# Kernel optimization log

Hardware: AMD Instinct MI355X
Metric: run time of the kernel (lower is better)

Reference implementation:

```python
import jax, jax.numpy as jnp
import numpy as np

N_NODES = 100000
N_EDGES = 200000
N_GRAPHS = 4000
F_IN = 44
H = 256
E = 512
L = 4


def setup_inputs() -> dict:
    key = jax.random.key(0)
    ks = jax.random.split(key, 16)
    x = jax.random.normal(ks[0], (N_NODES, F_IN), dtype=jnp.float32)
    edge_index = jax.random.randint(ks[1], (2, N_EDGES), 0, N_NODES)
    batch = jnp.sort(jax.random.randint(ks[2], (N_NODES,), 0, N_GRAPHS))
    s = lambda fan_in: 1.0 / np.sqrt(fan_in)
    W_atom = jax.random.uniform(ks[3], (F_IN, H), jnp.float32, -s(F_IN), s(F_IN))
    b_atom = jnp.zeros((H,), jnp.float32)
    W1 = jax.random.uniform(ks[4], (L, H, 2 * H), jnp.float32, -s(H), s(H))
    b1 = jnp.zeros((L, 2 * H), jnp.float32)
    W2 = jax.random.uniform(ks[5], (L, 2 * H, H), jnp.float32, -s(2 * H), s(2 * H))
    b2 = jnp.zeros((L, H), jnp.float32)
    Wf1 = jax.random.uniform(ks[6], (H, H), jnp.float32, -s(H), s(H))
    bf1 = jnp.zeros((H,), jnp.float32)
    Wf2 = jax.random.uniform(ks[7], (H, E), jnp.float32, -s(H), s(H))
    bf2 = jnp.zeros((E,), jnp.float32)
    return {"x": x, "edge_index": edge_index, "batch": batch,
            "W_atom": W_atom, "b_atom": b_atom,
            "W1": W1, "b1": b1, "W2": W2, "b2": b2,
            "Wf1": Wf1, "bf1": bf1, "Wf2": Wf2, "bf2": bf2}


def reference(x, edge_index, batch, W_atom, b_atom, W1, b1, W2, b2, Wf1, bf1, Wf2, bf2):
    src, dst = edge_index[0], edge_index[1]
    h = jax.nn.relu(x @ W_atom + b_atom)  # [N, H]
    for l in range(L):
        # GIN aggregation: agg_i = sum_{j->i} h_j ; eps=0 so node term is h_i itself
        agg = jax.ops.segment_sum(h[src], dst, num_segments=N_NODES)
        z = h + agg
        z = jax.nn.relu(z @ W1[l] + b1[l])
        z = z @ W2[l] + b2[l]
        h = jax.nn.relu(z)
    # global mean pool by graph id
    sums = jax.ops.segment_sum(h, batch, num_segments=N_GRAPHS)
    counts = jax.ops.segment_sum(jnp.ones((N_NODES,), h.dtype), batch, num_segments=N_GRAPHS)
    h_graph = sums / jnp.maximum(counts, 1.0)[:, None]  # [G, H]
    out = jax.nn.relu(h_graph @ Wf1 + bf1) @ Wf2 + bf2  # [G, E]
    return out
```

## Files before the change

### kernel.cpp

```cpp
#include <hip/hip_runtime.h>

#define N_NODES 100000
#define N_EDGES 200000
#define N_GRAPHS 4000
#define F_IN 44
#define HDIM 256
#define EDIM 512
#define NLAYERS 4

typedef float floatx4 __attribute__((ext_vector_type(4)));
typedef short bhalf8 __attribute__((ext_vector_type(8)));

__device__ __forceinline__ unsigned short f2bf(float f) {
    unsigned int u = __float_as_uint(f);
    u += 0x7FFFu + ((u >> 16) & 1u);
    return (unsigned short)(u >> 16);
}
__device__ __forceinline__ float bf2f(unsigned short s) {
    return __uint_as_float(((unsigned int)s) << 16);
}

__device__ __forceinline__ void gload16(const void* gsrc, void* ldst) {
    __builtin_amdgcn_global_load_lds(
        (const __attribute__((address_space(1))) void*)gsrc,
        (__attribute__((address_space(3))) void*)ldst, 16, 0, 0);
}

__global__ void zero_kernel(float* __restrict__ p, size_t n4) {
    size_t i = (size_t)blockIdx.x * blockDim.x + threadIdx.x;
    const size_t stride = (size_t)gridDim.x * blockDim.x;
    const float4 z = make_float4(0.f, 0.f, 0.f, 0.f);
    for (; i < n4; i += stride) ((float4*)p)[i] = z;
}

__global__ void xprep_kernel(const float* __restrict__ x, unsigned short* __restrict__ xb) {
    int idx = blockIdx.x * 256 + threadIdx.x;
    const int total = N_NODES * 16;
    const int stride = gridDim.x * 256;
    for (; idx < total; idx += stride) {
        const int n = idx >> 4, k4 = idx & 15;
        ushort4 v = make_ushort4(0, 0, 0, 0);
        if (k4 < F_IN / 4) {
            const float4 xv = *(const float4*)(x + (size_t)n * F_IN + k4 * 4);
            v.x = f2bf(xv.x); v.y = f2bf(xv.y); v.z = f2bf(xv.z); v.w = f2bf(xv.w);
        }
        *(ushort4*)(xb + (size_t)n * 64 + k4 * 4) = v;
    }
}

__global__ void hist_kernel(const int* __restrict__ dst, int* __restrict__ deg) {
    const int e = blockIdx.x * 256 + threadIdx.x;
    if (e < N_EDGES) atomicAdd(&deg[dst[e]], 1);
}

__global__ void scan1_kernel(const int* __restrict__ deg, int* __restrict__ row_ptr,
                             int* __restrict__ blk) {
    __shared__ int s[256];
    const int i = blockIdx.x * 256 + threadIdx.x;
    s[threadIdx.x] = (i < N_NODES) ? deg[i] : 0;
    __syncthreads();
    for (int off = 1; off < 256; off <<= 1) {
        int t = (threadIdx.x >= off) ? s[threadIdx.x - off] : 0;
        __syncthreads();
        s[threadIdx.x] += t;
        __syncthreads();
    }
    if (i < N_NODES) row_ptr[i + 1] = s[threadIdx.x];
    if (threadIdx.x == 255) blk[blockIdx.x] = s[255];
}

__global__ void scan2_kernel(int* __restrict__ blk, int nb) {
    if (threadIdx.x == 0 && blockIdx.x == 0) {
        int run = 0;
        for (int b = 0; b < nb; ++b) { const int t = blk[b]; blk[b] = run; run += t; }
    }
}

__global__ void scan3_kernel(int* __restrict__ row_ptr, const int* __restrict__ blk) {
    const int i = blockIdx.x * 256 + threadIdx.x;
    if (i < N_NODES) row_ptr[i + 1] += blk[i >> 8];
    if (i == 0) row_ptr[0] = 0;
}

__global__ void cursor_kernel(const int* __restrict__ row_ptr, int* __restrict__ cursor) {
    const int i = blockIdx.x * 256 + threadIdx.x;
    if (i < N_NODES) cursor[i] = row_ptr[i];
}

__global__ void fill_kernel(const int* __restrict__ src, const int* __restrict__ dst,
                            int* __restrict__ cursor, int* __restrict__ eids) {
    const int e = blockIdx.x * 256 + threadIdx.x;
    if (e < N_EDGES) {
        const int pos = atomicAdd(&cursor[dst[e]], 1);
        eids[pos] = src[e];
    }
}

__global__ void sort_kernel(const int* __restrict__ row_ptr, int* __restrict__ eids) {
    const int n = blockIdx.x * 256 + threadIdx.x;
    if (n < N_NODES) {
        const int s = row_ptr[n], e = row_ptr[n + 1];
        for (int i = s + 1; i < e; ++i) {
            const int v = eids[i];
            int j = i - 1;
            while (j >= s && eids[j] > v) { eids[j + 1] = eids[j]; --j; }
            eids[j + 1] = v;
        }
    }
}

__global__ void gather_kernel(const unsigned short* __restrict__ h,
                              const int* __restrict__ row_ptr,
                              const int* __restrict__ eids, unsigned short* __restrict__ z) {
    const int tid = threadIdx.x;
    const int n = blockIdx.x * 4 + (tid >> 6);
    const int t = tid & 63;
    const ushort4* h4 = (const ushort4*)h;
    ushort4 hv = h4[(size_t)n * 64 + t];
    float4 acc = make_float4(bf2f(hv.x), bf2f(hv.y), bf2f(hv.z), bf2f(hv.w));
    const int s = row_ptr[n], e = row_ptr[n + 1];
    for (int i = s; i < e; ++i) {
        const ushort4 v = h4[(size_t)eids[i] * 64 + t];
        acc.x += bf2f(v.x); acc.y += bf2f(v.y);
        acc.z += bf2f(v.z); acc.w += bf2f(v.w);
    }
    ushort4 pk;
    pk.x = f2bf(acc.x); pk.y = f2bf(acc.y);
    pk.z = f2bf(acc.z); pk.w = f2bf(acc.w);
    ((ushort4*)(z + (size_t)n * HDIM))[t] = pk;
}

__global__ void wprep_all(const float* __restrict__ W1, const float* __restrict__ W2,
                          const float* __restrict__ Wf1, const float* __restrict__ Wf2,
                          const float* __restrict__ Wa,
                          unsigned short* __restrict__ t1, unsigned short* __restrict__ t2,
                          unsigned short* __restrict__ tf1, unsigned short* __restrict__ tf2,
                          unsigned short* __restrict__ tat) {
    const int WSZ = HDIM * 2 * HDIM;
    const int T0 = 8 * WSZ;
    const int T1 = T0 + HDIM * HDIM;
    const int T2 = T1 + HDIM * EDIM;
    const int T3 = T2 + 64 * HDIM;
    const int stride = gridDim.x * 256;
    for (int idx = blockIdx.x * 256 + threadIdx.x; idx < T3; idx += stride) {
        if (idx < 4 * WSZ) {
            const int l = idx >> 17, e = idx & (WSZ - 1);
            const int k = e >> 9, n = e & 511;
            t1[(size_t)l * WSZ + n * HDIM + k] = f2bf(W1[idx]);
        } else if (idx < T0) {
            const int r = idx - 4 * WSZ;
            const int l = r >> 17, e = r & (WSZ - 1);
            const int k = e >> 8, n = e & 255;
            t2[(size_t)l * WSZ + n * EDIM + k] = f2bf(W2[r]);
        } else if (idx < T1) {
            const int e = idx - T0;
            const int k = e >> 8, n = e & 255;
            tf1[n * HDIM + k] = f2bf(Wf1[e]);
        } else if (idx < T2) {
            const int e = idx - T1;
            const int k = e >> 9, n = e & 511;
            tf2[n * HDIM + k] = f2bf(Wf2[e]);
        } else {
            const int e = idx - T2;
            const int n = e >> 6, k = e & 63;
            tat[n * 64 + k] = (k < F_IN) ? f2bf(Wa[k * HDIM + n]) : (unsigned short)0;
        }
    }
}

template <int OUT>
__global__ __launch_bounds__(256)
void gemm_mfma(const unsigned short* __restrict__ A, const unsigned short* __restrict__ BT,
               const float* __restrict__ bias, float* __restrict__ C,
               unsigned short* __restrict__ Z, int M, int N, int KK) {
    __shared__ __align__(16) unsigned short lds_all[32768];

    const int ncol = N >> 7;
    const int G = gridDim.x;
    int wg = blockIdx.x;
    {
        const int q = G >> 3, r = G & 7;
        const int xx = wg & 7, o = wg >> 3;
        wg = (xx < r ? xx * (q + 1) : r * (q + 1) + (xx - r) * q) + o;
    }
    const int col0 = (wg % ncol) << 7;
    const int row0 = (wg / ncol) << 7;

    const int tid = threadIdx.x;
    const int lane = tid & 63;
    const int w = tid >> 6;
    const int wr = w >> 1, wc = w & 1;
    const int lr = lane & 15;
    const int l4 = lane >> 4;

    const int srow = tid >> 3;
    const int sgran = ((tid & 7) ^ (srow & 7)) << 3;

    floatx4 acc[4][4];
#pragma unroll
    for (int m = 0; m < 4; ++m)
#pragma unroll
        for (int n = 0; n < 4; ++n) acc[m][n] = (floatx4){0.f, 0.f, 0.f, 0.f};

    const int NT = KK >> 6;

    auto stage = [&](int t, int b) {
        const int k0 = t << 6;
        unsigned short* la = &lds_all[b * 16384];
        unsigned short* lb = la + 8192;
#pragma unroll
        for (int pass = 0; pass < 4; ++pass) {
            const int r = (pass << 5) + srow;
            int ar = row0 + r; if (ar >= M) ar = M - 1;
            gload16(A + (size_t)ar * KK + k0 + sgran, &la[(pass << 11) + (w << 9)]);
            gload16(BT + (size_t)(col0 + r) * KK + k0 + sgran, &lb[(pass << 11) + (w << 9)]);
        }
    };

    stage(0, 0);
    if (NT > 1) stage(1, 1);
    for (int t = 0; t < NT; ++t) {
        const int cur = t & 1;
        if (t + 1 < NT) {
            asm volatile("s_waitcnt vmcnt(8)" ::: "memory");
        } else {
            asm volatile("s_waitcnt vmcnt(0)" ::: "memory");
        }
        __builtin_amdgcn_s_barrier();

        const unsigned short* la = &lds_all[cur * 16384];
        const unsigned short* lb = la + 8192;
#pragma unroll
        for (int s = 0; s < 2; ++s) {
            const int pg = (((s << 2) + l4) ^ (lr & 7)) << 3;
            bhalf8 fa[4], fb[4];
#pragma unroll
            for (int m = 0; m < 4; ++m)
                fa[m] = *(const bhalf8*)&la[((wr << 6) + (m << 4) + lr) * 64 + pg];
#pragma unroll
            for (int n = 0; n < 4; ++n)
                fb[n] = *(const bhalf8*)&lb[((wc << 6) + (n << 4) + lr) * 64 + pg];
#pragma unroll
            for (int m = 0; m < 4; ++m)
#pragma unroll
                for (int n = 0; n < 4; ++n)
                    acc[m][n] = __builtin_amdgcn_mfma_f32_16x16x32_bf16(fa[m], fb[n], acc[m][n], 0, 0, 0);
        }

        __builtin_amdgcn_s_barrier();
        if (t + 2 < NT) stage(t + 2, cur);
    }

    const int rgrp = l4 * 4;
    if (OUT == 2) {
        __syncthreads();
#pragma unroll
        for (int n = 0; n < 4; ++n) {
            const int colt = (wc << 6) + (n << 4) + lr;
            const float bv = bias[col0 + colt];
#pragma unroll
            for (int m = 0; m < 4; ++m) {
                const int rwt = (wr << 6) + (m << 4) + rgrp;
#pragma unroll
                for (int j = 0; j < 4; ++j)
                    lds_all[(rwt + j) * 136 + colt] = f2bf(fmaxf(acc[m][n][j] + bv, 0.f));
            }
        }
        __syncthreads();
        const int orow = tid >> 1;
        const int ocol = (tid & 1) << 6;
        if (row0 + orow < M) {
            const uint4* sp = (const uint4*)(lds_all + orow * 136 + ocol);
            uint4* dp = (uint4*)(Z + (size_t)(row0 + orow) * N + col0 + ocol);
#pragma unroll
            for (int q = 0; q < 8; ++q) dp[q] = sp[q];
        }
    } else {
#pragma unroll
        for (int n = 0; n < 4; ++n) {
            const int col = col0 + (wc << 6) + (n << 4) + lr;
            const float bv = bias[col];
#pragma unroll
            for (int m = 0; m < 4; ++m) {
                const int rw = row0 + (wr << 6) + (m << 4) + rgrp;
#pragma unroll
                for (int j = 0; j < 4; ++j) {
                    const int row = rw + j;
                    if (row < M) C[(size_t)row * N + col] = acc[m][n][j] + bv;
                }
            }
        }
    }
}

__global__ void pool_kernel(const unsigned short* __restrict__ h,
                            const int* __restrict__ batch,
                            unsigned short* __restrict__ gz) {
    __shared__ int sse[2];
    const int g = blockIdx.x;
    if (threadIdx.x < 2) {
        const int target = g + threadIdx.x;
        int lo = 0, hi = N_NODES;
        while (lo < hi) {
            const int mid = (lo + hi) >> 1;
            if (batch[mid] < target) lo = mid + 1; else hi = mid;
        }
        sse[threadIdx.x] = lo;
    }
    __syncthreads();
    const int s = sse[0], e = sse[1];
    const int j = threadIdx.x;
    float acc = 0.f;
    for (int n = s; n < e; ++n) acc += bf2f(h[(size_t)n * HDIM + j]);
    const float v = acc * ((e > s) ? 1.f / (float)(e - s) : 1.f);
    gz[(size_t)g * HDIM + j] = f2bf(v);
}

extern "C" void kernel_launch(void* const* d_in, const int* in_sizes, int n_in,
                              void* d_out, int out_size, void* d_ws, size_t ws_size,
                              hipStream_t stream) {
    const float* x      = (const float*)d_in[0];
    const int*   eidx   = (const int*)d_in[1];
    const int*   batch  = (const int*)d_in[2];
    const float* W_atom = (const float*)d_in[3];
    const float* b_atom = (const float*)d_in[4];
    const float* W1     = (const float*)d_in[5];
    const float* b1     = (const float*)d_in[6];
    const float* W2     = (const float*)d_in[7];
    const float* b2     = (const float*)d_in[8];
    const float* Wf1    = (const float*)d_in[9];
    const float* bf1    = (const float*)d_in[10];
    const float* Wf2    = (const float*)d_in[11];
    const float* bf2    = (const float*)d_in[12];
    float* out = (float*)d_out;

    const int* src = eidx;
    const int* dst = eidx + N_EDGES;

    const size_t NH = (size_t)N_NODES * HDIM;
    const int WSZ = HDIM * 2 * HDIM;

    char* base = (char*)d_ws;
    size_t off = 0;
    unsigned short* h = (unsigned short*)(base + off);      off += NH * 2;
    unsigned short* zin = (unsigned short*)(base + off);    off += NH * 2;
    unsigned short* xb = (unsigned short*)(base + off);     off += (size_t)N_NODES * 64 * 2;
    int* deg     = (int*)(base + off);            off += (size_t)N_NODES * 4;
    int* row_ptr = (int*)(base + off);            off += (size_t)(N_NODES + 1) * 4;
    int* cursor  = (int*)(base + off);            off += (size_t)N_NODES * 4;
    int* eids    = (int*)(base + off);            off += (size_t)N_EDGES * 4;
    int* blk     = (int*)(base + off);            off += 512 * 4;
    off = (off + 255) & ~(size_t)255;
    unsigned short* t1 = (unsigned short*)(base + off); off += (size_t)NLAYERS * WSZ * 2;
    unsigned short* t2 = (unsigned short*)(base + off); off += (size_t)NLAYERS * WSZ * 2;
    unsigned short* tf1 = (unsigned short*)(base + off); off += (size_t)HDIM * HDIM * 2;
    unsigned short* tf2 = (unsigned short*)(base + off); off += (size_t)HDIM * EDIM * 2;
    unsigned short* tat = (unsigned short*)(base + off); off += (size_t)HDIM * 64 * 2;
    off = (off + 255) & ~(size_t)255;

    const size_t avail = (ws_size > off) ? ws_size - off : 0;
    long chunk = (long)(avail / ((size_t)EDIM * 2));
    if (chunk >= N_NODES) chunk = N_NODES;
    else chunk &= ~127L;
    if (chunk < 128) chunk = 128;
    unsigned short* z2 = (unsigned short*)(base + off);

    const size_t GH = (size_t)N_GRAPHS * HDIM;
    unsigned short* hg  = zin;
    unsigned short* hg1 = zin + GH;

    const int nb = (N_NODES + 255) / 256;

    xprep_kernel<<<1024, 256, 0, stream>>>(x, xb);
    wprep_all<<<1024, 256, 0, stream>>>(W1, W2, Wf1, Wf2, W_atom, t1, t2, tf1, tf2, tat);

    zero_kernel<<<128, 256, 0, stream>>>((float*)deg, N_NODES / 4);
    hist_kernel<<<(N_EDGES + 255) / 256, 256, 0, stream>>>(dst, deg);
    scan1_kernel<<<nb, 256, 0, stream>>>(deg, row_ptr, blk);
    scan2_kernel<<<1, 64, 0, stream>>>(blk, nb);
    scan3_kernel<<<nb, 256, 0, stream>>>(row_ptr, blk);
    cursor_kernel<<<nb, 256, 0, stream>>>(row_ptr, cursor);
    fill_kernel<<<(N_EDGES + 255) / 256, 256, 0, stream>>>(src, dst, cursor, eids);
    sort_kernel<<<nb, 256, 0, stream>>>(row_ptr, eids);

    {
        const int nrow1 = (N_NODES + 127) / 128;
        gemm_mfma<2><<<2 * nrow1, 256, 0, stream>>>(
            xb, tat, b_atom, nullptr, h, N_NODES, HDIM, 64);
    }

    for (int l = 0; l < NLAYERS; ++l) {
        gather_kernel<<<N_NODES / 4, 256, 0, stream>>>(h, row_ptr, eids, zin);
        for (long r0 = 0; r0 < N_NODES; r0 += chunk) {
            const int mc = (int)((N_NODES - r0 < chunk) ? (N_NODES - r0) : chunk);
            const int nrow1 = (mc + 127) / 128;
            gemm_mfma<2><<<4 * nrow1, 256, 0, stream>>>(
                zin + (size_t)r0 * HDIM, t1 + (size_t)l * WSZ,
                b1 + (size_t)l * 2 * HDIM, nullptr, z2, mc, 2 * HDIM, HDIM);
            gemm_mfma<2><<<2 * nrow1, 256, 0, stream>>>(
                z2, t2 + (size_t)l * WSZ,
                b2 + (size_t)l * HDIM, nullptr, h + (size_t)r0 * HDIM, mc, HDIM, 2 * HDIM);
        }
    }

    pool_kernel<<<N_GRAPHS, HDIM, 0, stream>>>(h, batch, hg);

    gemm_mfma<2><<<2 * ((N_GRAPHS + 127) / 128), 256, 0, stream>>>(
        hg, tf1, bf1, nullptr, hg1, N_GRAPHS, HDIM, HDIM);
    gemm_mfma<0><<<4 * ((N_GRAPHS + 127) / 128), 256, 0, stream>>>(
        hg1, tf2, bf2, out, nullptr, N_GRAPHS, EDIM, HDIM);
}
```

Measured before the change: 762.8 us.

## Fuse per-layer two-GEMM MLP into one kernel keeping intermediate in LDS

Replaces the two back-to-back MFMA GEMM launches per GIN layer with a single fused kernel. Each 128-row block computes the 512-wide hidden activation in 64-column chunks, stores each chunk in LDS after bias and ReLU, and immediately accumulates it into the 256-wide output. This removes the global write and re-read of the 100000x512 bf16 intermediate buffer and the chunking logic that depended on workspace size. In exchange it uses a large per-thread accumulator (128 floats) and about 74KB of LDS per block. It also has only one block per 128 rows with no double buffering, so occupancy and load/compute overlap may suffer.

```diff
diff --git a/kernel.cpp b/kernel.cpp
--- a/kernel.cpp
+++ b/kernel.cpp
@@ -168,6 +168,145 @@
     }
 }
 
+__global__ __launch_bounds__(256, 2)
+void fused_layer(const unsigned short* __restrict__ zin, const unsigned short* __restrict__ T1,
+                 const unsigned short* __restrict__ T2, const float* __restrict__ b1,
+                 const float* __restrict__ b2, unsigned short* __restrict__ H, int M) {
+    __shared__ __align__(16) unsigned short lds[37888];
+    unsigned short* sA  = lds;
+    unsigned short* sB1 = lds + 8192;
+    unsigned short* zb  = lds + 12288;
+    unsigned short* sB2 = lds + 21504;
+
+    const int G = gridDim.x;
+    int wg = blockIdx.x;
+    {
+        const int q = G >> 3, r = G & 7;
+        const int xx = wg & 7, o = wg >> 3;
+        wg = (xx < r ? xx * (q + 1) : r * (q + 1) + (xx - r) * q) + o;
+    }
+    const int row0 = wg << 7;
+
+    const int tid = threadIdx.x;
+    const int lane = tid & 63;
+    const int w = tid >> 6;
+    const int wr = w >> 1, wc = w & 1;
+    const int lr = lane & 15;
+    const int l4 = lane >> 4;
+    const int rgrp = l4 * 4;
+    const int srow = tid >> 3;
+    const int sgran = ((tid & 7) ^ (srow & 7)) << 3;
+
+    floatx4 acc_h[4][8];
+#pragma unroll
+    for (int m = 0; m < 4; ++m)
+#pragma unroll
+        for (int n = 0; n < 8; ++n) acc_h[m][n] = (floatx4){0.f, 0.f, 0.f, 0.f};
+
+#pragma unroll 1
+    for (int c = 0; c < 8; ++c) {
+        floatx4 acc_z[4][2];
+#pragma unroll
+        for (int m = 0; m < 4; ++m)
+#pragma unroll
+            for (int n = 0; n < 2; ++n) acc_z[m][n] = (floatx4){0.f, 0.f, 0.f, 0.f};
+
+#pragma unroll 1
+        for (int t = 0; t < 4; ++t) {
+            __syncthreads();
+#pragma unroll
+            for (int p = 0; p < 4; ++p) {
+                const int r = (p << 5) + srow;
+                int ar = row0 + r; if (ar >= M) ar = M - 1;
+                gload16(zin + (size_t)ar * 256 + (t << 6) + sgran, &sA[(p << 11) + (w << 9)]);
+            }
+#pragma unroll
+            for (int p = 0; p < 2; ++p) {
+                const int r = (p << 5) + srow;
+                gload16(T1 + (size_t)((c << 6) + r) * 256 + (t << 6) + sgran,
+                        &sB1[(p << 11) + (w << 9)]);
+            }
+            __syncthreads();
+#pragma unroll
+            for (int s = 0; s < 2; ++s) {
+                const int pg = (((s << 2) + l4) ^ (lr & 7)) << 3;
+                bhalf8 fa[4], fb[2];
+#pragma unroll
+                for (int m = 0; m < 4; ++m)
+                    fa[m] = *(const bhalf8*)&sA[((wr << 6) + (m << 4) + lr) * 64 + pg];
+#pragma unroll
+                for (int n = 0; n < 2; ++n)
+                    fb[n] = *(const bhalf8*)&sB1[((wc << 5) + (n << 4) + lr) * 64 + pg];
+#pragma unroll
+                for (int m = 0; m < 4; ++m)
+#pragma unroll
+                    for (int n = 0; n < 2; ++n)
+                        acc_z[m][n] = __builtin_amdgcn_mfma_f32_16x16x32_bf16(fa[m], fb[n], acc_z[m][n], 0, 0, 0);
+            }
+        }
+
+#pragma unroll
+        for (int n = 0; n < 2; ++n) {
+            const int ck = (wc << 5) + (n << 4) + lr;
+            const float bv = b1[(c << 6) + ck];
+#pragma unroll
+            for (int m = 0; m < 4; ++m) {
+                const int rw = (wr << 6) + (m << 4) + rgrp;
+#pragma unroll
+                for (int j = 0; j < 4; ++j)
+                    zb[(rw + j) * 72 + ck] = f2bf(fmaxf(acc_z[m][n][j] + bv, 0.f));
+            }
+        }
+#pragma unroll
+        for (int p = 0; p < 8; ++p) {
+            const int r = (p << 5) + srow;
+            gload16(T2 + (size_t)r * 512 + (c << 6) + sgran, &sB2[(p << 11) + (w << 9)]);
+        }
+        __syncthreads();
+
+#pragma unroll
+        for (int s = 0; s < 2; ++s) {
+            const int pg = (((s << 2) + l4) ^ (lr & 7)) << 3;
+            const int zg = ((s << 2) + l4) << 3;
+            bhalf8 fa[4], fb[8];
+#pragma unroll
+            for (int m = 0; m < 4; ++m)
+                fa[m] = *(const bhalf8*)&zb[((wr << 6) + (m << 4) + lr) * 72 + zg];
+#pragma unroll
+            for (int n = 0; n < 8; ++n)
+                fb[n] = *(const bhalf8*)&sB2[((wc << 7) + (n << 4) + lr) * 64 + pg];
+#pragma unroll
+            for (int m = 0; m < 4; ++m)
+#pragma unroll
+                for (int n = 0; n < 8; ++n)
+                    acc_h[m][n] = __builtin_amdgcn_mfma_f32_16x16x32_bf16(fa[m], fb[n], acc_h[m][n], 0, 0, 0);
+        }
+    }
+
+    __syncthreads();
+#pragma unroll
+    for (int n = 0; n < 8; ++n) {
+        const int colt = (wc << 7) + (n << 4) + lr;
+        const float bv = b2[colt];
+#pragma unroll
+        for (int m = 0; m < 4; ++m) {
+            const int rwt = (wr << 6) + (m << 4) + rgrp;
+#pragma unroll
+            for (int j = 0; j < 4; ++j)
+                lds[(rwt + j) * 264 + colt] = f2bf(fmaxf(acc_h[m][n][j] + bv, 0.f));
+        }
+    }
+    __syncthreads();
+    const int orow = tid >> 1;
+    const int ohalf = (tid & 1) << 7;
+    if (row0 + orow < M) {
+        const uint4* sp = (const uint4*)(lds + orow * 264 + ohalf);
+        uint4* dp = (uint4*)(H + (size_t)(row0 + orow) * 256 + ohalf);
+#pragma unroll
+        for (int q = 0; q < 16; ++q) dp[q] = sp[q];
+    }
+}
+
 template <int OUT>
 __global__ __launch_bounds__(256)
 void gemm_mfma(const unsigned short* __restrict__ A, const unsigned short* __restrict__ BT,
@@ -192,7 +331,6 @@
     const int wr = w >> 1, wc = w & 1;
     const int lr = lane & 15;
     const int l4 = lane >> 4;
-
     const int srow = tid >> 3;
     const int sgran = ((tid & 7) ^ (srow & 7)) << 3;
 
@@ -358,18 +496,12 @@
     unsigned short* tat = (unsigned short*)(base + off); off += (size_t)HDIM * 64 * 2;
     off = (off + 255) & ~(size_t)255;
 
-    const size_t avail = (ws_size > off) ? ws_size - off : 0;
-    long chunk = (long)(avail / ((size_t)EDIM * 2));
-    if (chunk >= N_NODES) chunk = N_NODES;
-    else chunk &= ~127L;
-    if (chunk < 128) chunk = 128;
-    unsigned short* z2 = (unsigned short*)(base + off);
-
     const size_t GH = (size_t)N_GRAPHS * HDIM;
     unsigned short* hg  = zin;
     unsigned short* hg1 = zin + GH;
 
     const int nb = (N_NODES + 255) / 256;
+    const int nrow128 = (N_NODES + 127) / 128;
 
     xprep_kernel<<<1024, 256, 0, stream>>>(x, xb);
     wprep_all<<<1024, 256, 0, stream>>>(W1, W2, Wf1, Wf2, W_atom, t1, t2, tf1, tf2, tat);
@@ -383,24 +515,14 @@
     fill_kernel<<<(N_EDGES + 255) / 256, 256, 0, stream>>>(src, dst, cursor, eids);
     sort_kernel<<<nb, 256, 0, stream>>>(row_ptr, eids);
 
-    {
-        const int nrow1 = (N_NODES + 127) / 128;
-        gemm_mfma<2><<<2 * nrow1, 256, 0, stream>>>(
-            xb, tat, b_atom, nullptr, h, N_NODES, HDIM, 64);
-    }
+    gemm_mfma<2><<<2 * nrow128, 256, 0, stream>>>(
+        xb, tat, b_atom, nullptr, h, N_NODES, HDIM, 64);
 
     for (int l = 0; l < NLAYERS; ++l) {
         gather_kernel<<<N_NODES / 4, 256, 0, stream>>>(h, row_ptr, eids, zin);
-        for (long r0 = 0; r0 < N_NODES; r0 += chunk) {
-            const int mc = (int)((N_NODES - r0 < chunk) ? (N_NODES - r0) : chunk);
-            const int nrow1 = (mc + 127) / 128;
-            gemm_mfma<2><<<4 * nrow1, 256, 0, stream>>>(
-                zin + (size_t)r0 * HDIM, t1 + (size_t)l * WSZ,
-                b1 + (size_t)l * 2 * HDIM, nullptr, z2, mc, 2 * HDIM, HDIM);
-            gemm_mfma<2><<<2 * nrow1, 256, 0, stream>>>(
-                z2, t2 + (size_t)l * WSZ,
-                b2 + (size_t)l * HDIM, nullptr, h + (size_t)r0 * HDIM, mc, HDIM, 2 * HDIM);
-        }
+        fused_layer<<<nrow128, 256, 0, stream>>>(
+            zin, t1 + (size_t)l * WSZ, t2 + (size_t)l * WSZ,
+            b1 + (size_t)l * 2 * HDIM, b2 + (size_t)l * HDIM, h, N_NODES);
     }
 
     pool_kernel<<<N_GRAPHS, HDIM, 0, stream>>>(h, batch, hg);
```

Result: no change. 749.0 us (median of 2 runs) (-1.8%).

## Make MFMA GEMM persistent with cross-tile pipelined K-stage loads

Applied to the files above, without the earlier changes.

Turns the per-tile GEMM into a persistent kernel: each block walks several contiguous output tiles as one flattened stream of K-steps, so loads for the next tile are prefetched while the current tile's epilogue runs. The grid is capped at 512 blocks and K is made a template parameter so index math is resolved at compile time. The epilogue is rewritten to reuse the just-consumed LDS buffer in two half-tile passes. The intent is to remove per-block prologue and tail costs and to overlap memory with compute across tile boundaries, at the price of extra barriers in the epilogue and possible load imbalance from the fixed tiles-per-block split.

```diff
diff --git a/kernel.cpp b/kernel.cpp
--- a/kernel.cpp
+++ b/kernel.cpp
@@ -168,23 +168,28 @@
     }
 }
 
-template <int OUT>
+template <int OUT, int NT>
 __global__ __launch_bounds__(256)
-void gemm_mfma(const unsigned short* __restrict__ A, const unsigned short* __restrict__ BT,
-               const float* __restrict__ bias, float* __restrict__ C,
-               unsigned short* __restrict__ Z, int M, int N, int KK) {
-    __shared__ __align__(16) unsigned short lds_all[32768];
+void gemm_mt(const unsigned short* __restrict__ A, const unsigned short* __restrict__ BT,
+             const float* __restrict__ bias, float* __restrict__ C,
+             unsigned short* __restrict__ Z, int M, int N, int tpb) {
+    constexpr int KK = NT * 64;
+    __shared__ __align__(16) unsigned short lds[32768];
 
     const int ncol = N >> 7;
+    const int nrow = (M + 127) >> 7;
+    const int ntile = nrow * ncol;
     const int G = gridDim.x;
-    int wg = blockIdx.x;
+    int b = blockIdx.x;
     {
         const int q = G >> 3, r = G & 7;
-        const int xx = wg & 7, o = wg >> 3;
-        wg = (xx < r ? xx * (q + 1) : r * (q + 1) + (xx - r) * q) + o;
-    }
-    const int col0 = (wg % ncol) << 7;
-    const int row0 = (wg / ncol) << 7;
+        const int xx = b & 7, o = b >> 3;
+        b = (xx < r ? xx * (q + 1) : r * (q + 1) + (xx - r) * q) + o;
+    }
+    const int tile0 = b * tpb;
+    if (tile0 >= ntile) return;
+    const int tend = (tile0 + tpb < ntile) ? tile0 + tpb : ntile;
+    const int S = (tend - tile0) * NT;
 
     const int tid = threadIdx.x;
     const int lane = tid & 63;
@@ -192,47 +197,53 @@
     const int wr = w >> 1, wc = w & 1;
     const int lr = lane & 15;
     const int l4 = lane >> 4;
-
+    const int rgrp = l4 * 4;
     const int srow = tid >> 3;
     const int sgran = ((tid & 7) ^ (srow & 7)) << 3;
 
-    floatx4 acc[4][4];
-#pragma unroll
-    for (int m = 0; m < 4; ++m)
-#pragma unroll
-        for (int n = 0; n < 4; ++n) acc[m][n] = (floatx4){0.f, 0.f, 0.f, 0.f};
-
-    const int NT = KK >> 6;
-
-    auto stage = [&](int t, int b) {
+    auto stage = [&](int s) {
+        const int tau = tile0 + s / NT;
+        const int t = s % NT;
+        const int r0 = (tau / ncol) << 7;
+        const int c0 = (tau % ncol) << 7;
         const int k0 = t << 6;
-        unsigned short* la = &lds_all[b * 16384];
+        unsigned short* la = &lds[(s & 1) * 16384];
         unsigned short* lb = la + 8192;
 #pragma unroll
         for (int pass = 0; pass < 4; ++pass) {
             const int r = (pass << 5) + srow;
-            int ar = row0 + r; if (ar >= M) ar = M - 1;
+            int ar = r0 + r; if (ar >= M) ar = M - 1;
             gload16(A + (size_t)ar * KK + k0 + sgran, &la[(pass << 11) + (w << 9)]);
-            gload16(BT + (size_t)(col0 + r) * KK + k0 + sgran, &lb[(pass << 11) + (w << 9)]);
+            gload16(BT + (size_t)(c0 + r) * KK + k0 + sgran, &lb[(pass << 11) + (w << 9)]);
         }
     };
 
-    stage(0, 0);
-    if (NT > 1) stage(1, 1);
-    for (int t = 0; t < NT; ++t) {
-        const int cur = t & 1;
-        if (t + 1 < NT) {
+    floatx4 acc[4][4];
+#pragma unroll
+    for (int m = 0; m < 4; ++m)
+#pragma unroll
+        for (int n = 0; n < 4; ++n) acc[m][n] = (floatx4){0.f, 0.f, 0.f, 0.f};
+
+    stage(0);
+    if (S > 1) stage(1);
+    for (int s = 0; s < S; ++s) {
+        const int tau = tile0 + s / NT;
+        const int t = s % NT;
+        const int row0 = (tau / ncol) << 7;
+        const int col0 = (tau % ncol) << 7;
+
+        if (s + 1 < S) {
             asm volatile("s_waitcnt vmcnt(8)" ::: "memory");
         } else {
             asm volatile("s_waitcnt vmcnt(0)" ::: "memory");
         }
         __builtin_amdgcn_s_barrier();
 
-        const unsigned short* la = &lds_all[cur * 16384];
+        const unsigned short* la = &lds[(s & 1) * 16384];
         const unsigned short* lb = la + 8192;
 #pragma unroll
-        for (int s = 0; s < 2; ++s) {
-            const int pg = (((s << 2) + l4) ^ (lr & 7)) << 3;
+        for (int ss = 0; ss < 2; ++ss) {
+            const int pg = (((ss << 2) + l4) ^ (lr & 7)) << 3;
             bhalf8 fa[4], fb[4];
 #pragma unroll
             for (int m = 0; m < 4; ++m)
@@ -247,49 +258,65 @@
                     acc[m][n] = __builtin_amdgcn_mfma_f32_16x16x32_bf16(fa[m], fb[n], acc[m][n], 0, 0, 0);
         }
 
+        asm volatile("s_waitcnt lgkmcnt(0)" ::: "memory");
         __builtin_amdgcn_s_barrier();
-        if (t + 2 < NT) stage(t + 2, cur);
-    }
-
-    const int rgrp = l4 * 4;
-    if (OUT == 2) {
-        __syncthreads();
-#pragma unroll
-        for (int n = 0; n < 4; ++n) {
-            const int colt = (wc << 6) + (n << 4) + lr;
-            const float bv = bias[col0 + colt];
-#pragma unroll
-            for (int m = 0; m < 4; ++m) {
-                const int rwt = (wr << 6) + (m << 4) + rgrp;
-#pragma unroll
-                for (int j = 0; j < 4; ++j)
-                    lds_all[(rwt + j) * 136 + colt] = f2bf(fmaxf(acc[m][n][j] + bv, 0.f));
-            }
-        }
-        __syncthreads();
-        const int orow = tid >> 1;
-        const int ocol = (tid & 1) << 6;
-        if (row0 + orow < M) {
-            const uint4* sp = (const uint4*)(lds_all + orow * 136 + ocol);
-            uint4* dp = (uint4*)(Z + (size_t)(row0 + orow) * N + col0 + ocol);
-#pragma unroll
-            for (int q = 0; q < 8; ++q) dp[q] = sp[q];
-        }
-    } else {
-#pragma unroll
-        for (int n = 0; n < 4; ++n) {
-            const int col = col0 + (wc << 6) + (n << 4) + lr;
-            const float bv = bias[col];
-#pragma unroll
-            for (int m = 0; m < 4; ++m) {
-                const int rw = row0 + (wr << 6) + (m << 4) + rgrp;
-#pragma unroll
-                for (int j = 0; j < 4; ++j) {
-                    const int row = rw + j;
-                    if (row < M) C[(size_t)row * N + col] = acc[m][n][j] + bv;
+
+        if (t == NT - 1) {
+            unsigned short* scratch = &lds[(s & 1) * 16384];
+            if (OUT == 2) {
+#pragma unroll
+                for (int half = 0; half < 2; ++half) {
+                    if (wr == half) {
+#pragma unroll
+                        for (int n = 0; n < 4; ++n) {
+                            const int colt = (wc << 6) + (n << 4) + lr;
+                            const float bv = bias[col0 + colt];
+#pragma unroll
+                            for (int m = 0; m < 4; ++m) {
+#pragma unroll
+                                for (int j = 0; j < 4; ++j)
+                                    scratch[((m << 4) + rgrp + j) * 136 + colt] =
+                                        f2bf(fmaxf(acc[m][n][j] + bv, 0.f));
+                            }
+                        }
+                    }
+                    asm volatile("s_waitcnt lgkmcnt(0)" ::: "memory");
+                    __builtin_amdgcn_s_barrier();
+                    const int orow = tid >> 2;
+                    const int oc = (tid & 3) << 5;
+                    const int grow = row0 + (half << 6) + orow;
+                    if (grow < M) {
+                        const uint4* sp = (const uint4*)(scratch + orow * 136 + oc);
+                        uint4* dp = (uint4*)(Z + (size_t)grow * N + col0 + oc);
+#pragma unroll
+                        for (int q = 0; q < 4; ++q) dp[q] = sp[q];
+                    }
+                    asm volatile("s_waitcnt lgkmcnt(0)" ::: "memory");
+                    __builtin_amdgcn_s_barrier();
+                }
+            } else {
+#pragma unroll
+                for (int n = 0; n < 4; ++n) {
+                    const int col = col0 + (wc << 6) + (n << 4) + lr;
+                    const float bv = bias[col];
+#pragma unroll
+                    for (int m = 0; m < 4; ++m) {
+                        const int rw = row0 + (wr << 6) + (m << 4) + rgrp;
+#pragma unroll
+                        for (int j = 0; j < 4; ++j) {
+                            const int row = rw + j;
+                            if (row < M) C[(size_t)row * N + col] = acc[m][n][j] + bv;
+                        }
+                    }
                 }
             }
-        }
+#pragma unroll
+            for (int m = 0; m < 4; ++m)
+#pragma unroll
+                for (int n = 0; n < 4; ++n) acc[m][n] = (floatx4){0.f, 0.f, 0.f, 0.f};
+        }
+
+        if (s + 2 < S) stage(s + 2);
     }
 }
 
@@ -370,6 +397,13 @@
     unsigned short* hg1 = zin + GH;
 
     const int nb = (N_NODES + 255) / 256;
+    const int NBLK_MAX = 512;
+
+    auto launch_cfg = [&](int M, int N, int& nblk, int& tpb) {
+        const int ntile = ((M + 127) / 128) * (N / 128);
+        nblk = (ntile < NBLK_MAX) ? ntile : NBLK_MAX;
+        tpb = (ntile + nblk - 1) / nblk;
+    };
 
     xprep_kernel<<<1024, 256, 0, stream>>>(x, xb);
     wprep_all<<<1024, 256, 0, stream>>>(W1, W2, Wf1, Wf2, W_atom, t1, t2, tf1, tf2, tat);
@@ -384,29 +418,35 @@
     sort_kernel<<<nb, 256, 0, stream>>>(row_ptr, eids);
 
     {
-        const int nrow1 = (N_NODES + 127) / 128;
-        gemm_mfma<2><<<2 * nrow1, 256, 0, stream>>>(
-            xb, tat, b_atom, nullptr, h, N_NODES, HDIM, 64);
+        int nblk, tpb; launch_cfg(N_NODES, HDIM, nblk, tpb);
+        gemm_mt<2, 1><<<nblk, 256, 0, stream>>>(
+            xb, tat, b_atom, nullptr, h, N_NODES, HDIM, tpb);
     }
 
     for (int l = 0; l < NLAYERS; ++l) {
         gather_kernel<<<N_NODES / 4, 256, 0, stream>>>(h, row_ptr, eids, zin);
         for (long r0 = 0; r0 < N_NODES; r0 += chunk) {
             const int mc = (int)((N_NODES - r0 < chunk) ? (N_NODES - r0) : chunk);
-            const int nrow1 = (mc + 127) / 128;
-            gemm_mfma<2><<<4 * nrow1, 256, 0, stream>>>(
+            int nblk, tpb;
+            launch_cfg(mc, 2 * HDIM, nblk, tpb);
+            gemm_mt<2, 4><<<nblk, 256, 0, stream>>>(
                 zin + (size_t)r0 * HDIM, t1 + (size_t)l * WSZ,
-                b1 + (size_t)l * 2 * HDIM, nullptr, z2, mc, 2 * HDIM, HDIM);
-            gemm_mfma<2><<<2 * nrow1, 256, 0, stream>>>(
+                b1 + (size_t)l * 2 * HDIM, nullptr, z2, mc, 2 * HDIM, tpb);
+            launch_cfg(mc, HDIM, nblk, tpb);
+            gemm_mt<2, 8><<<nblk, 256, 0, stream>>>(
                 z2, t2 + (size_t)l * WSZ,
-                b2 + (size_t)l * HDIM, nullptr, h + (size_t)r0 * HDIM, mc, HDIM, 2 * HDIM);
+                b2 + (size_t)l * HDIM, nullptr, h + (size_t)r0 * HDIM, mc, HDIM, tpb);
         }
     }
 
     pool_kernel<<<N_GRAPHS, HDIM, 0, stream>>>(h, batch, hg);
 
-    gemm_mfma<2><<<2 * ((N_GRAPHS + 127) / 128), 256, 0, stream>>>(
-        hg, tf1, bf1, nullptr, hg1, N_GRAPHS, HDIM, HDIM);
-    gemm_mfma<0><<<4 * ((N_GRAPHS + 127) / 128), 256, 0, stream>>>(
-        hg1, tf2, bf2, out, nullptr, N_GRAPHS, EDIM, HDIM);
-}
+    {
+        int nblk, tpb; launch_cfg(N_GRAPHS, HDIM, nblk, tpb);
+        gemm_mt<2, 4><<<nblk, 256, 0, stream>>>(
+            hg, tf1, bf1, nullptr, hg1, N_GRAPHS, HDIM, tpb);
+        launch_cfg(N_GRAPHS, EDIM, nblk, tpb);
+        gemm_mt<0, 4><<<nblk, 256, 0, stream>>>(
+            hg1, tf2, bf2, out, nullptr, N_GRAPHS, EDIM, tpb);
+    }
+}
```

After: 902.8 us. 18.4% more time.
